# Kernel tuning notes

Hardware: AMD Instinct MI355X
Metric: run time of the kernel (lower is better)

## Reference

```python
import jax, jax.numpy as jnp
import numpy as np

B, S, H = 2, 2048, 1024
NUM_HEAD = 16
HEAD_HIDDEN = H // NUM_HEAD
SCALE = float(np.sqrt(HEAD_HIDDEN))  # 8.0
INF = 10000000000.0


def setup_inputs() -> dict:
    key = jax.random.key(0)
    ks = jax.random.split(key, 12)
    std = 1.0 / np.sqrt(H)
    mk = lambda k: (jax.random.normal(k, (H, H), jnp.float32) * std)
    return {
        "query": jax.random.normal(ks[0], (B, S, H), jnp.float32),
        "key": jax.random.normal(ks[1], (B, S, H), jnp.float32),
        "value": jax.random.normal(ks[2], (B, S, H), jnp.float32),
        "att_mask": jnp.ones((B, 1, 1, S), jnp.float32),
        "wq": mk(ks[3]), "bq": jnp.zeros((H,), jnp.float32),
        "wk": mk(ks[4]), "bk": jnp.zeros((H,), jnp.float32),
        "wv": mk(ks[5]), "bv": jnp.zeros((H,), jnp.float32),
        "wo": mk(ks[6]), "bo": jnp.zeros((H,), jnp.float32),
    }


def reference(query, key, value, att_mask, wq, bq, wk, bk, wv, bv, wo, bo):
    # projections (weights stored as [in, out])
    q = query @ wq + bq
    k = key @ wk + bk
    v = value @ wv + bv
    # split heads: [B, S, nH, hd]
    q = q.reshape(B, S, NUM_HEAD, HEAD_HIDDEN)
    k = k.reshape(B, S, NUM_HEAD, HEAD_HIDDEN)
    v = v.reshape(B, S, NUM_HEAD, HEAD_HIDDEN)
    # scores [B, nH, Sq, Sk], first divide by scale
    att = jnp.einsum("bqhd,bkhd->bhqk", q, k) / SCALE
    # additive mask applied BEFORE the second scale division (faithful quirk)
    att = att + (1.0 - att_mask) * (-INF)
    att = jax.nn.softmax(att / SCALE, axis=-1)
    out = jnp.einsum("bhqk,bkhd->bqhd", att, v).reshape(B, S, H)
    return out @ wo + bo
```

## Files before the change

kernel.cpp:

```cpp
#include <hip/hip_runtime.h>
#include <cstdint>

typedef unsigned short u16;
typedef __attribute__((ext_vector_type(8))) short bf16x8;
typedef __attribute__((ext_vector_type(4))) short bf16x4;
typedef __attribute__((ext_vector_type(4))) float f32x4;

#define S_LEN 2048
#define HDIM  1024
#define NHEAD 16

__device__ __forceinline__ float bf2f(u16 u){ return __uint_as_float(((uint32_t)u) << 16); }
__device__ __forceinline__ u16 f2bf(float f){
  uint32_t x = __float_as_uint(f);
  return (u16)((x + 0x7fffu + ((x >> 16) & 1u)) >> 16);
}

__device__ __forceinline__ float exp2_fast(float x){
  float r; asm("v_exp_f32 %0, %1" : "=v"(r) : "v"(x)); return r;
}

__device__ __forceinline__ void gload_lds16(const void* g, void* l){
  __builtin_amdgcn_global_load_lds((const __attribute__((address_space(1))) void*)g,
                                   (__attribute__((address_space(3))) void*)l, 16, 0, 0);
}

__global__ __launch_bounds__(256) void k_cvt3(const float* __restrict__ q, const float* __restrict__ k,
                                              const float* __restrict__ v, u16* __restrict__ oq,
                                              u16* __restrict__ ok, u16* __restrict__ ov){
  int z = blockIdx.y;
  const float* in = z == 0 ? q : (z == 1 ? k : v);
  u16* out = z == 0 ? oq : (z == 1 ? ok : ov);
  int i = blockIdx.x * 256 + threadIdx.x;
  float4 f0 = *(const float4*)&in[(size_t)i * 8];
  float4 f1 = *(const float4*)&in[(size_t)i * 8 + 4];
  bf16x8 o;
  o[0] = (short)f2bf(f0.x); o[1] = (short)f2bf(f0.y);
  o[2] = (short)f2bf(f0.z); o[3] = (short)f2bf(f0.w);
  o[4] = (short)f2bf(f1.x); o[5] = (short)f2bf(f1.y);
  o[6] = (short)f2bf(f1.z); o[7] = (short)f2bf(f1.w);
  *(bf16x8*)&out[(size_t)i * 8] = o;
}

__global__ __launch_bounds__(256) void k_tr_w4(const float* __restrict__ w0, const float* __restrict__ w1,
                                               const float* __restrict__ w2, const float* __restrict__ w3,
                                               u16* __restrict__ o0, u16* __restrict__ o1,
                                               u16* __restrict__ o2, u16* __restrict__ o3){
  int z = blockIdx.z;
  const float* in = z == 0 ? w0 : (z == 1 ? w1 : (z == 2 ? w2 : w3));
  u16* out = z == 0 ? o0 : (z == 1 ? o1 : (z == 2 ? o2 : o3));
  __shared__ float t[64][65];
  int r0 = threadIdx.x >> 6;
  int c  = threadIdx.x & 63;
  int bx = blockIdx.x * 64, by = blockIdx.y * 64;
  #pragma unroll
  for (int i = 0; i < 64; i += 4) t[r0 + i][c] = in[(size_t)(by + r0 + i) * 1024 + bx + c];
  __syncthreads();
  #pragma unroll
  for (int i = 0; i < 64; i += 4) out[(size_t)(bx + r0 + i) * 1024 + by + c] = f2bf(t[c][r0 + i]);
}

__global__ __launch_bounds__(256) void k_tr_v(const u16* __restrict__ v, u16* __restrict__ vt){
  __shared__ u16 t[64][65];
  int r0 = threadIdx.x >> 6, c = threadIdx.x & 63;
  int s0 = blockIdx.x * 64;
  int bh = blockIdx.y;
  int b = bh >> 4, h = bh & 15;
  const u16* src = v + (size_t)b * S_LEN * HDIM + h * 64;
  #pragma unroll
  for (int i = 0; i < 64; i += 4) t[r0 + i][c] = src[(size_t)(s0 + r0 + i) * HDIM + c];
  __syncthreads();
  u16* dst = vt + (size_t)bh * 64 * S_LEN + s0;
  #pragma unroll
  for (int i = 0; i < 64; i += 4) dst[(size_t)(r0 + i) * S_LEN + c] = t[c][r0 + i];
}

__global__ __launch_bounds__(256) void k_gemm_qkv(const u16* __restrict__ A0, const u16* __restrict__ A1,
                                                  const u16* __restrict__ A2,
                                                  const u16* __restrict__ W0, const u16* __restrict__ W1,
                                                  const u16* __restrict__ W2,
                                                  const float* __restrict__ b0, const float* __restrict__ b1,
                                                  const float* __restrict__ b2,
                                                  u16* __restrict__ C0, u16* __restrict__ C1,
                                                  u16* __restrict__ C2)
{
  int z = blockIdx.z;
  const u16* A  = z == 0 ? A0 : (z == 1 ? A1 : A2);
  const u16* Wt = z == 0 ? W0 : (z == 1 ? W1 : W2);
  const float* bias = z == 0 ? b0 : (z == 1 ? b1 : b2);
  u16* C = z == 0 ? C0 : (z == 1 ? C1 : C2);
  float scale = z == 0 ? (1.44269504f / 64.0f) : 1.0f;

  __shared__ u16 As[128 * 32];
  __shared__ u16 Bs[128 * 32];
  const int K = 1024, N = 1024;
  int tid = threadIdx.x;
  int lane = tid & 63, wave = tid >> 6;
  int quad = lane >> 4, c16 = lane & 15;
  int wm = wave >> 1, wn = wave & 1;
  int m0 = blockIdx.x * 128, n0 = blockIdx.y * 128;

  f32x4 acc[4][4] = {};

  for (int k0 = 0; k0 < K; k0 += 32) {
    #pragma unroll
    for (int i = 0; i < 2; i++) {
      int slot = tid + i * 256;
      int r = slot >> 2, cc = (slot & 3) * 8;
      gload_lds16(&A [(size_t)(m0 + r) * K + k0 + cc], &As[slot * 8]);
      gload_lds16(&Wt[(size_t)(n0 + r) * K + k0 + cc], &Bs[slot * 8]);
    }
    __syncthreads();
    bf16x8 af[4], bfr[4];
    #pragma unroll
    for (int mt = 0; mt < 4; mt++) af[mt]  = *(const bf16x8*)&As[(wm * 64 + mt * 16 + c16) * 32 + quad * 8];
    #pragma unroll
    for (int nt = 0; nt < 4; nt++) bfr[nt] = *(const bf16x8*)&Bs[(wn * 64 + nt * 16 + c16) * 32 + quad * 8];
    #pragma unroll
    for (int mt = 0; mt < 4; mt++)
      #pragma unroll
      for (int nt = 0; nt < 4; nt++)
        acc[mt][nt] = __builtin_amdgcn_mfma_f32_16x16x32_bf16(af[mt], bfr[nt], acc[mt][nt], 0, 0, 0);
    __syncthreads();
  }

  #pragma unroll
  for (int nt = 0; nt < 4; nt++) {
    int gc = n0 + wn * 64 + nt * 16 + c16;
    float bv = bias[gc];
    #pragma unroll
    for (int mt = 0; mt < 4; mt++)
      #pragma unroll
      for (int r = 0; r < 4; r++) {
        int gr = m0 + wm * 64 + mt * 16 + quad * 4 + r;
        C[(size_t)gr * N + gc] = f2bf((acc[mt][nt][r] + bv) * scale);
      }
  }
}

__global__ __launch_bounds__(256) void k_gemm_o(const u16* __restrict__ A, const u16* __restrict__ Wt,
                                                const float* __restrict__ bias, float* __restrict__ C)
{
  __shared__ u16 As[128 * 32];
  __shared__ u16 Bs[64 * 32];
  const int K = 1024, N = 1024;
  int tid = threadIdx.x;
  int lane = tid & 63, wave = tid >> 6;
  int quad = lane >> 4, c16 = lane & 15;
  int wm = wave >> 1, wn = wave & 1;
  int m0 = blockIdx.x * 128, n0 = blockIdx.y * 64;

  f32x4 acc[4][2] = {};

  for (int k0 = 0; k0 < K; k0 += 32) {
    #pragma unroll
    for (int i = 0; i < 2; i++) {
      int slot = tid + i * 256;
      int r = slot >> 2, cc = (slot & 3) * 8;
      gload_lds16(&A[(size_t)(m0 + r) * K + k0 + cc], &As[slot * 8]);
    }
    {
      int r = tid >> 2, cc = (tid & 3) * 8;
      gload_lds16(&Wt[(size_t)(n0 + r) * K + k0 + cc], &Bs[tid * 8]);
    }
    __syncthreads();
    bf16x8 af[4], bfr[2];
    #pragma unroll
    for (int mt = 0; mt < 4; mt++) af[mt]  = *(const bf16x8*)&As[(wm * 64 + mt * 16 + c16) * 32 + quad * 8];
    #pragma unroll
    for (int nt = 0; nt < 2; nt++) bfr[nt] = *(const bf16x8*)&Bs[(wn * 32 + nt * 16 + c16) * 32 + quad * 8];
    #pragma unroll
    for (int mt = 0; mt < 4; mt++)
      #pragma unroll
      for (int nt = 0; nt < 2; nt++)
        acc[mt][nt] = __builtin_amdgcn_mfma_f32_16x16x32_bf16(af[mt], bfr[nt], acc[mt][nt], 0, 0, 0);
    __syncthreads();
  }

  #pragma unroll
  for (int nt = 0; nt < 2; nt++) {
    int gc = n0 + wn * 32 + nt * 16 + c16;
    float bv = bias[gc];
    #pragma unroll
    for (int mt = 0; mt < 4; mt++)
      #pragma unroll
      for (int r = 0; r < 4; r++) {
        int gr = m0 + wm * 64 + mt * 16 + quad * 4 + r;
        C[(size_t)gr * N + gc] = acc[mt][nt][r] + bv;
      }
  }
}

__global__ __launch_bounds__(256, 2) void k_attn(const u16* __restrict__ Qm,
                                                 const u16* __restrict__ Km,
                                                 const u16* __restrict__ VTm,
                                                 const float* __restrict__ mask,
                                                 u16* __restrict__ Om)
{
  __shared__ u16 KV[2][9216];
  __shared__ float Msall[S_LEN];
  const int NT = S_LEN / 64;
  int tid = threadIdx.x;
  int lane = tid & 63, wave = tid >> 6;
  int quad = lane >> 4, c16 = lane & 15;
  int wq = wave >> 1, wkv = wave & 1;
  int qb = blockIdx.x, h = blockIdx.y, b = blockIdx.z;
  const size_t SH = (size_t)S_LEN * HDIM;
  const u16* Qbase  = Qm + (size_t)b * SH + (size_t)qb * 128 * HDIM + h * 64;
  const u16* Kbase  = Km + (size_t)b * SH + h * 64;
  const u16* VTbase = VTm + (size_t)(b * NHEAD + h) * 64 * S_LEN;
  const float* Mbase = mask + (size_t)b * S_LEN;

  auto stage = [&](int s0, int bb) {
    #pragma unroll
    for (int i = 0; i < 5; i++) {
      int c = i * 256 + tid;
      if (c < 576) {
        int r = c / 9, cc = c - r * 9;
        int col = (cc == 8) ? 0 : cc * 8;
        gload_lds16(&Kbase[(size_t)(s0 + r) * HDIM + col], &KV[bb][c * 8]);
      } else if (c < 1152) {
        int c2 = c - 576;
        int r = c2 / 9, cc = c2 - r * 9;
        int col = (cc == 8) ? 0 : cc * 8;
        gload_lds16(&VTbase[(size_t)r * S_LEN + s0 + col], &KV[bb][4608 + c2 * 8]);
      }
    }
  };

  stage(0, 0);
  for (int i = tid; i < S_LEN; i += 256) Msall[i] = (1.0f - Mbase[i]) * (-1.8033688e9f);

  int qw0 = wq * 64;
  int kv0 = wkv * 32;

  bf16x8 bq[4][2];
  #pragma unroll
  for (int qt = 0; qt < 4; qt++)
    #pragma unroll
    for (int kk = 0; kk < 2; kk++)
      bq[qt][kk] = *(const bf16x8*)&Qbase[(size_t)(qw0 + qt * 16 + c16) * HDIM + kk * 32 + quad * 8];

  f32x4 oacc[4][4] = {};
  float lsq[4] = {};

  __syncthreads();

  for (int kt = 0; kt < NT; kt++) {
    int s0 = kt * 64;
    int cb = kt & 1;
    const u16* Kb = &KV[cb][0];
    const u16* Vb = &KV[cb][4608];
    if (kt + 1 < NT) stage(s0 + 64, cb ^ 1);

    f32x4 madd[2];
    #pragma unroll
    for (int kv2 = 0; kv2 < 2; kv2++) madd[kv2] = *(const f32x4*)&Msall[s0 + kv0 + kv2 * 16 + quad * 4];

    bf16x8 ak0[2], ak1[2];
    #pragma unroll
    for (int kv2 = 0; kv2 < 2; kv2++) {
      ak0[kv2] = *(const bf16x8*)&Kb[(kv0 + kv2 * 16 + c16) * 72 + quad * 8];
      ak1[kv2] = *(const bf16x8*)&Kb[(kv0 + kv2 * 16 + c16) * 72 + 32 + quad * 8];
    }
    f32x4 sacc[2][4];
    __builtin_amdgcn_s_setprio(1);
    #pragma unroll
    for (int kv2 = 0; kv2 < 2; kv2++)
      #pragma unroll
      for (int qt = 0; qt < 4; qt++)
        sacc[kv2][qt] = __builtin_amdgcn_mfma_f32_16x16x32_bf16(ak0[kv2], bq[qt][0], madd[kv2], 0, 0, 0);
    #pragma unroll
    for (int kv2 = 0; kv2 < 2; kv2++)
      #pragma unroll
      for (int qt = 0; qt < 4; qt++)
        sacc[kv2][qt] = __builtin_amdgcn_mfma_f32_16x16x32_bf16(ak1[kv2], bq[qt][1], sacc[kv2][qt], 0, 0, 0);
    __builtin_amdgcn_s_setprio(0);

    bf16x4 pa[4][2];
    #pragma unroll
    for (int kv2 = 0; kv2 < 2; kv2++)
      #pragma unroll
      for (int qt = 0; qt < 4; qt++) {
        float p0 = exp2_fast(sacc[kv2][qt][0]);
        float p1 = exp2_fast(sacc[kv2][qt][1]);
        float p2 = exp2_fast(sacc[kv2][qt][2]);
        float p3 = exp2_fast(sacc[kv2][qt][3]);
        lsq[qt] += (p0 + p1) + (p2 + p3);
        union { uint32_t u[2]; bf16x4 v; } cv;
        asm("v_cvt_pk_bf16_f32 %0, %1, %2" : "=v"(cv.u[0]) : "v"(p0), "v"(p1));
        asm("v_cvt_pk_bf16_f32 %0, %1, %2" : "=v"(cv.u[1]) : "v"(p2), "v"(p3));
        pa[qt][kv2] = cv.v;
      }

    __builtin_amdgcn_s_setprio(1);
    #pragma unroll
    for (int kv2 = 0; kv2 < 2; kv2++) {
      bf16x4 vb[4];
      #pragma unroll
      for (int dt = 0; dt < 4; dt++)
        vb[dt] = *(const bf16x4*)&Vb[(dt * 16 + c16) * 72 + kv0 + kv2 * 16 + quad * 4];
      #pragma unroll
      for (int qt = 0; qt < 4; qt++)
        #pragma unroll
        for (int dt = 0; dt < 4; dt++)
          oacc[qt][dt] = __builtin_amdgcn_mfma_f32_16x16x16bf16_1k(pa[qt][kv2], vb[dt], oacc[qt][dt], 0, 0, 0);
    }
    __builtin_amdgcn_s_setprio(0);
    __syncthreads();
  }

  #pragma unroll
  for (int qt = 0; qt < 4; qt++) {
    float v = lsq[qt];
    v += __shfl_xor(v, 16);
    v += __shfl_xor(v, 32);
    lsq[qt] = v;
  }

  float* Osc = (float*)&KV[0][0];
  float* Lsc = Msall;
  if (wkv == 1) {
    float* Ob = Osc + wq * 4096;
    #pragma unroll
    for (int qt = 0; qt < 4; qt++)
      #pragma unroll
      for (int dt = 0; dt < 4; dt++)
        #pragma unroll
        for (int r = 0; r < 4; r++)
          Ob[(qt * 16 + quad * 4 + r) * 64 + dt * 16 + c16] = oacc[qt][dt][r];
    if (lane < 16)
      #pragma unroll
      for (int qt = 0; qt < 4; qt++) Lsc[wq * 64 + qt * 16 + lane] = lsq[qt];
  }
  __syncthreads();
  if (wkv == 0) {
    float* Ob = Osc + wq * 4096;
    u16* Obase = Om + (size_t)b * SH + (size_t)qb * 128 * HDIM + h * 64;
    #pragma unroll
    for (int qt = 0; qt < 4; qt++)
      #pragma unroll
      for (int r = 0; r < 4; r++) {
        float l = __shfl(lsq[qt], quad * 4 + r) + Lsc[wq * 64 + qt * 16 + quad * 4 + r];
        float rinv = 1.0f / l;
        int lr = qw0 + qt * 16 + quad * 4 + r;
        #pragma unroll
        for (int dt = 0; dt < 4; dt++) {
          float o = oacc[qt][dt][r] + Ob[(qt * 16 + quad * 4 + r) * 64 + dt * 16 + c16];
          Obase[(size_t)lr * HDIM + dt * 16 + c16] = f2bf(o * rinv);
        }
      }
  }
}

extern "C" void kernel_launch(void* const* d_in, const int* in_sizes, int n_in,
                              void* d_out, int out_size, void* d_ws, size_t ws_size,
                              hipStream_t stream)
{
  (void)in_sizes; (void)n_in; (void)out_size; (void)ws_size;
  const float* q_in = (const float*)d_in[0];
  const float* k_in = (const float*)d_in[1];
  const float* v_in = (const float*)d_in[2];
  const float* mask = (const float*)d_in[3];
  const float* wq   = (const float*)d_in[4];
  const float* bq   = (const float*)d_in[5];
  const float* wk   = (const float*)d_in[6];
  const float* bk   = (const float*)d_in[7];
  const float* wv   = (const float*)d_in[8];
  const float* bv   = (const float*)d_in[9];
  const float* wo   = (const float*)d_in[10];
  const float* bo   = (const float*)d_in[11];

  u16* ws  = (u16*)d_ws;
  u16* wqt = ws;
  u16* wkt = wqt + (1u << 20);
  u16* wvt = wkt + (1u << 20);
  u16* wot = wvt + (1u << 20);
  u16* qi_ = wot + (1u << 20);
  u16* ki_ = qi_ + (4u << 20);
  u16* vi_ = ki_ + (4u << 20);
  u16* qb_ = vi_ + (4u << 20);
  u16* kb_ = qb_ + (4u << 20);
  u16* vb_ = kb_ + (4u << 20);
  u16* vtb = vb_ + (4u << 20);
  u16* ob_ = vtb + (4u << 20);

  dim3 blk(256);
  k_cvt3<<<dim3(2048, 3), blk, 0, stream>>>(q_in, k_in, v_in, qi_, ki_, vi_);
  k_tr_w4<<<dim3(16, 16, 4), blk, 0, stream>>>(wq, wk, wv, wo, wqt, wkt, wvt, wot);
  k_gemm_qkv<<<dim3(32, 8, 3), blk, 0, stream>>>(qi_, ki_, vi_, wqt, wkt, wvt, bq, bk, bv, qb_, kb_, vb_);
  k_tr_v<<<dim3(32, 32), blk, 0, stream>>>(vb_, vtb);
  k_attn<<<dim3(16, 16, 2), blk, 0, stream>>>(qb_, kb_, vtb, mask, ob_);
  k_gemm_o<<<dim3(32, 16), blk, 0, stream>>>(ob_, wot, bo, (float*)d_out);
}
```

Measured before the change: 226.1 us.

## Merge input conversion kernels and fuse V transpose into QKV GEMM epilogue

Combines the fp32-to-bf16 activation conversion and weight transpose kernels into a single launch. The V projection GEMM now writes its output already transposed per head through an LDS staging tile, which removes the separate V transpose kernel and its extra global round trip. This cuts two kernel launches and one 8 MB read/write pass. In exchange it adds LDS use and barriers in the GEMM epilogue for the z==2 blocks, which may reduce occupancy of the QKV GEMM.

```diff
diff --git a/kernel.cpp b/kernel.cpp
--- a/kernel.cpp
+++ b/kernel.cpp
@@ -25,54 +25,42 @@
                                    (__attribute__((address_space(3))) void*)l, 16, 0, 0);
 }
 
-__global__ __launch_bounds__(256) void k_cvt3(const float* __restrict__ q, const float* __restrict__ k,
-                                              const float* __restrict__ v, u16* __restrict__ oq,
-                                              u16* __restrict__ ok, u16* __restrict__ ov){
-  int z = blockIdx.y;
-  const float* in = z == 0 ? q : (z == 1 ? k : v);
-  u16* out = z == 0 ? oq : (z == 1 ? ok : ov);
-  int i = blockIdx.x * 256 + threadIdx.x;
-  float4 f0 = *(const float4*)&in[(size_t)i * 8];
-  float4 f1 = *(const float4*)&in[(size_t)i * 8 + 4];
-  bf16x8 o;
-  o[0] = (short)f2bf(f0.x); o[1] = (short)f2bf(f0.y);
-  o[2] = (short)f2bf(f0.z); o[3] = (short)f2bf(f0.w);
-  o[4] = (short)f2bf(f1.x); o[5] = (short)f2bf(f1.y);
-  o[6] = (short)f2bf(f1.z); o[7] = (short)f2bf(f1.w);
-  *(bf16x8*)&out[(size_t)i * 8] = o;
-}
-
-__global__ __launch_bounds__(256) void k_tr_w4(const float* __restrict__ w0, const float* __restrict__ w1,
-                                               const float* __restrict__ w2, const float* __restrict__ w3,
-                                               u16* __restrict__ o0, u16* __restrict__ o1,
-                                               u16* __restrict__ o2, u16* __restrict__ o3){
-  int z = blockIdx.z;
-  const float* in = z == 0 ? w0 : (z == 1 ? w1 : (z == 2 ? w2 : w3));
-  u16* out = z == 0 ? o0 : (z == 1 ? o1 : (z == 2 ? o2 : o3));
+__global__ __launch_bounds__(256) void k_pre(const float* __restrict__ q, const float* __restrict__ k,
+                                             const float* __restrict__ v, u16* __restrict__ oq,
+                                             u16* __restrict__ ok, u16* __restrict__ ov,
+                                             const float* __restrict__ w0, const float* __restrict__ w1,
+                                             const float* __restrict__ w2, const float* __restrict__ w3,
+                                             u16* __restrict__ o0, u16* __restrict__ o1,
+                                             u16* __restrict__ o2, u16* __restrict__ o3)
+{
   __shared__ float t[64][65];
-  int r0 = threadIdx.x >> 6;
-  int c  = threadIdx.x & 63;
-  int bx = blockIdx.x * 64, by = blockIdx.y * 64;
-  #pragma unroll
-  for (int i = 0; i < 64; i += 4) t[r0 + i][c] = in[(size_t)(by + r0 + i) * 1024 + bx + c];
-  __syncthreads();
-  #pragma unroll
-  for (int i = 0; i < 64; i += 4) out[(size_t)(bx + r0 + i) * 1024 + by + c] = f2bf(t[c][r0 + i]);
-}
-
-__global__ __launch_bounds__(256) void k_tr_v(const u16* __restrict__ v, u16* __restrict__ vt){
-  __shared__ u16 t[64][65];
-  int r0 = threadIdx.x >> 6, c = threadIdx.x & 63;
-  int s0 = blockIdx.x * 64;
-  int bh = blockIdx.y;
-  int b = bh >> 4, h = bh & 15;
-  const u16* src = v + (size_t)b * S_LEN * HDIM + h * 64;
-  #pragma unroll
-  for (int i = 0; i < 64; i += 4) t[r0 + i][c] = src[(size_t)(s0 + r0 + i) * HDIM + c];
-  __syncthreads();
-  u16* dst = vt + (size_t)bh * 64 * S_LEN + s0;
-  #pragma unroll
-  for (int i = 0; i < 64; i += 4) dst[(size_t)(r0 + i) * S_LEN + c] = t[c][r0 + i];
+  int bid = blockIdx.x, tid = threadIdx.x;
+  if (bid < 6144) {
+    int z = bid / 2048, xi = bid - z * 2048;
+    const float* in = z == 0 ? q : (z == 1 ? k : v);
+    u16* out = z == 0 ? oq : (z == 1 ? ok : ov);
+    int i = xi * 256 + tid;
+    float4 f0 = *(const float4*)&in[(size_t)i * 8];
+    float4 f1 = *(const float4*)&in[(size_t)i * 8 + 4];
+    bf16x8 o;
+    o[0] = (short)f2bf(f0.x); o[1] = (short)f2bf(f0.y);
+    o[2] = (short)f2bf(f0.z); o[3] = (short)f2bf(f0.w);
+    o[4] = (short)f2bf(f1.x); o[5] = (short)f2bf(f1.y);
+    o[6] = (short)f2bf(f1.z); o[7] = (short)f2bf(f1.w);
+    *(bf16x8*)&out[(size_t)i * 8] = o;
+  } else {
+    int wid = bid - 6144;
+    int z = wid >> 8, rem = wid & 255;
+    int by = (rem >> 4) * 64, bx = (rem & 15) * 64;
+    const float* in = z == 0 ? w0 : (z == 1 ? w1 : (z == 2 ? w2 : w3));
+    u16* out = z == 0 ? o0 : (z == 1 ? o1 : (z == 2 ? o2 : o3));
+    int r0 = tid >> 6, c = tid & 63;
+    #pragma unroll
+    for (int i = 0; i < 64; i += 4) t[r0 + i][c] = in[(size_t)(by + r0 + i) * 1024 + bx + c];
+    __syncthreads();
+    #pragma unroll
+    for (int i = 0; i < 64; i += 4) out[(size_t)(bx + r0 + i) * 1024 + by + c] = f2bf(t[c][r0 + i]);
+  }
 }
 
 __global__ __launch_bounds__(256) void k_gemm_qkv(const u16* __restrict__ A0, const u16* __restrict__ A1,
@@ -82,17 +70,17 @@
                                                   const float* __restrict__ b0, const float* __restrict__ b1,
                                                   const float* __restrict__ b2,
                                                   u16* __restrict__ C0, u16* __restrict__ C1,
-                                                  u16* __restrict__ C2)
+                                                  u16* __restrict__ vt)
 {
   int z = blockIdx.z;
   const u16* A  = z == 0 ? A0 : (z == 1 ? A1 : A2);
   const u16* Wt = z == 0 ? W0 : (z == 1 ? W1 : W2);
   const float* bias = z == 0 ? b0 : (z == 1 ? b1 : b2);
-  u16* C = z == 0 ? C0 : (z == 1 ? C1 : C2);
   float scale = z == 0 ? (1.44269504f / 64.0f) : 1.0f;
 
   __shared__ u16 As[128 * 32];
   __shared__ u16 Bs[128 * 32];
+  __shared__ u16 T[64 * 136];
   const int K = 1024, N = 1024;
   int tid = threadIdx.x;
   int lane = tid & 63, wave = tid >> 6;
@@ -124,17 +112,49 @@
     __syncthreads();
   }
 
-  #pragma unroll
-  for (int nt = 0; nt < 4; nt++) {
-    int gc = n0 + wn * 64 + nt * 16 + c16;
-    float bv = bias[gc];
-    #pragma unroll
-    for (int mt = 0; mt < 4; mt++)
-      #pragma unroll
-      for (int r = 0; r < 4; r++) {
-        int gr = m0 + wm * 64 + mt * 16 + quad * 4 + r;
-        C[(size_t)gr * N + gc] = f2bf((acc[mt][nt][r] + bv) * scale);
-      }
+  if (z == 2) {
+    int b_ = m0 >> 11;
+    int s_base = m0 & 2047;
+    #pragma unroll
+    for (int p = 0; p < 2; p++) {
+      if (wn == p) {
+        #pragma unroll
+        for (int nt = 0; nt < 4; nt++) {
+          float bv2 = bias[n0 + p * 64 + nt * 16 + c16];
+          #pragma unroll
+          for (int mt = 0; mt < 4; mt++) {
+            union { u16 u[4]; uint64_t qw; } pk;
+            #pragma unroll
+            for (int r = 0; r < 4; r++) pk.u[r] = f2bf(acc[mt][nt][r] + bv2);
+            *(uint64_t*)&T[(nt * 16 + c16) * 136 + wm * 64 + mt * 16 + quad * 4] = pk.qw;
+          }
+        }
+      }
+      __syncthreads();
+      {
+        int d = tid >> 2, ch = tid & 3;
+        int hh = (n0 >> 6) + p;
+        u16* vrow = vt + ((size_t)(b_ * 16 + hh) * 64 + d) * S_LEN + s_base + ch * 32;
+        #pragma unroll
+        for (int j = 0; j < 4; j++)
+          *(bf16x8*)&vrow[j * 8] = *(const bf16x8*)&T[d * 136 + ch * 32 + j * 8];
+      }
+      __syncthreads();
+    }
+  } else {
+    u16* C = z == 0 ? C0 : C1;
+    #pragma unroll
+    for (int nt = 0; nt < 4; nt++) {
+      int gc = n0 + wn * 64 + nt * 16 + c16;
+      float bv2 = bias[gc];
+      #pragma unroll
+      for (int mt = 0; mt < 4; mt++)
+        #pragma unroll
+        for (int r = 0; r < 4; r++) {
+          int gr = m0 + wm * 64 + mt * 16 + quad * 4 + r;
+          C[(size_t)gr * N + gc] = f2bf((acc[mt][nt][r] + bv2) * scale);
+        }
+    }
   }
 }
 
@@ -180,13 +200,13 @@
   #pragma unroll
   for (int nt = 0; nt < 2; nt++) {
     int gc = n0 + wn * 32 + nt * 16 + c16;
-    float bv = bias[gc];
+    float bv2 = bias[gc];
     #pragma unroll
     for (int mt = 0; mt < 4; mt++)
       #pragma unroll
       for (int r = 0; r < 4; r++) {
         int gr = m0 + wm * 64 + mt * 16 + quad * 4 + r;
-        C[(size_t)gr * N + gc] = acc[mt][nt][r] + bv;
+        C[(size_t)gr * N + gc] = acc[mt][nt][r] + bv2;
       }
   }
 }
@@ -386,10 +406,10 @@
   u16* ob_ = vtb + (4u << 20);
 
   dim3 blk(256);
-  k_cvt3<<<dim3(2048, 3), blk, 0, stream>>>(q_in, k_in, v_in, qi_, ki_, vi_);
-  k_tr_w4<<<dim3(16, 16, 4), blk, 0, stream>>>(wq, wk, wv, wo, wqt, wkt, wvt, wot);
-  k_gemm_qkv<<<dim3(32, 8, 3), blk, 0, stream>>>(qi_, ki_, vi_, wqt, wkt, wvt, bq, bk, bv, qb_, kb_, vb_);
-  k_tr_v<<<dim3(32, 32), blk, 0, stream>>>(vb_, vtb);
+  k_pre<<<dim3(7168), blk, 0, stream>>>(q_in, k_in, v_in, qi_, ki_, vi_,
+                                        wq, wk, wv, wo, wqt, wkt, wvt, wot);
+  k_gemm_qkv<<<dim3(32, 8, 3), blk, 0, stream>>>(qi_, ki_, vi_, wqt, wkt, wvt, bq, bk, bv,
+                                                 qb_, kb_, vtb);
   k_attn<<<dim3(16, 16, 2), blk, 0, stream>>>(qb_, kb_, vtb, mask, ob_);
   k_gemm_o<<<dim3(32, 16), blk, 0, stream>>>(ob_, wot, bo, (float*)d_out);
 }
```

New measurement: 235.8 us. 4.3% more time.
